# Optimization experiments

Measured on AMD Instinct MI355X. Metric: run time of the kernel, lower is better.

The kernel has to match this reference:

```python
import jax, jax.numpy as jnp
import numpy as np

# ---- config (matches init_kwargs) ----
B, N, D = 16, 300, 256
HEADS, HD = 8, D // 8
FF = 1024
HID = FF // 2                      # SwiGLU hidden
SPATIAL = [(80, 80), (40, 40), (20, 20), (10, 10)]
LVL = len(SPATIAL)
NP = 4                              # points per level
TP = LVL * NP                       # total sampling points = 16
L = sum(h * w for h, w in SPATIAL)  # 8400
EPS = 1e-6


def setup_inputs() -> dict:
    key = jax.random.key(0)
    ks = jax.random.split(key, 24)
    s = 0.02
    return {
        "target": jax.random.normal(ks[0], (B, N, D), jnp.float32),
        "reference_points": jax.random.uniform(ks[1], (B, N, 1, 4), jnp.float32, 0.05, 0.95),
        "memory": jax.random.normal(ks[2], (B, L, D), jnp.float32),
        # self-attention
        "qkv_w": jax.random.normal(ks[3], (3 * D, D), jnp.float32) * s,
        "qkv_b": jnp.zeros((3 * D,), jnp.float32),
        "out_w": jax.random.normal(ks[4], (D, D), jnp.float32) * s,
        "out_b": jnp.zeros((D,), jnp.float32),
        "norm1_w": jnp.ones((D,), jnp.float32),
        # deformable cross-attention
        "off_w": jax.random.normal(ks[5], (HEADS * TP * 2, D), jnp.float32) * s,
        "off_b": jax.random.normal(ks[6], (HEADS * TP * 2,), jnp.float32) * 0.1,
        "aw_w": jax.random.normal(ks[7], (HEADS * TP, D), jnp.float32) * s,
        "aw_b": jnp.zeros((HEADS * TP,), jnp.float32),
        "cout_w": jax.random.normal(ks[8], (D, D), jnp.float32) * s,
        "cout_b": jnp.zeros((D,), jnp.float32),
        "norm2_w": jnp.ones((D,), jnp.float32),
        # SwiGLU FFN
        "w13": jax.random.normal(ks[9], (2 * HID, D), jnp.float32) * s,
        "w13_b": jnp.zeros((2 * HID,), jnp.float32),
        "w2": jax.random.normal(ks[10], (D, HID), jnp.float32) * s,
        "w2_b": jnp.zeros((D,), jnp.float32),
        "norm3_w": jnp.ones((D,), jnp.float32),
    }


def rmsnorm(x, w):
    return x * jax.lax.rsqrt(jnp.mean(x * x, axis=-1, keepdims=True) + EPS) * w


def bilinear_sample(vflat, loc, H, W):
    """vflat: (BH, hd, H*W); loc: (BH, Q, 2) in [0,1]. grid_sample align_corners=False, zero pad."""
    x = loc[..., 0] * W - 0.5
    y = loc[..., 1] * H - 0.5
    x0 = jnp.floor(x); y0 = jnp.floor(y)
    dx = x - x0; dy = y - y0
    x0i = x0.astype(jnp.int32); y0i = y0.astype(jnp.int32)

    def gather(xi, yi, w):
        valid = (xi >= 0) & (xi < W) & (yi >= 0) & (yi < H)
        idx = jnp.clip(yi, 0, H - 1) * W + jnp.clip(xi, 0, W - 1)
        g = jnp.take_along_axis(vflat, idx[:, None, :], axis=2)  # (BH, hd, Q)
        return g * (w * valid)[:, None, :]

    return (gather(x0i, y0i, (1 - dx) * (1 - dy))
            + gather(x0i + 1, y0i, dx * (1 - dy))
            + gather(x0i, y0i + 1, (1 - dx) * dy)
            + gather(x0i + 1, y0i + 1, dx * dy))


def reference(target, reference_points, memory, qkv_w, qkv_b, out_w, out_b, norm1_w,
              off_w, off_b, aw_w, aw_b, cout_w, cout_b, norm2_w,
              w13, w13_b, w2, w2_b, norm3_w):
    # ---------- self-attention (query_pos_embed=None, attn_mask=None) ----------
    qkv = target @ qkv_w.T + qkv_b                    # (B,N,3D)
    qkv = qkv.reshape(B, N, 3, HEADS, HD).transpose(2, 0, 3, 1, 4)
    q, k, v = qkv[0], qkv[1], qkv[2]                  # (B,H,N,hd)
    attn = jax.nn.softmax(jnp.einsum("bhqd,bhkd->bhqk", q, k) / np.sqrt(HD), axis=-1)
    sa = jnp.einsum("bhqk,bhkd->bhqd", attn, v).transpose(0, 2, 1, 3).reshape(B, N, D)
    x = rmsnorm(target + (sa @ out_w.T + out_b), norm1_w)

    # ---------- deformable cross-attention ----------
    # value_op: memory -> per-head value (B,H,hd,L)
    val = memory.reshape(B, L, HEADS, HD).transpose(0, 2, 3, 1).reshape(B * HEADS, HD, L)

    offsets = (x @ off_w.T + off_b).reshape(B, N, HEADS, TP, 2)
    aw = jax.nn.softmax((x @ aw_w.T + aw_b).reshape(B, N, HEADS, TP), axis=-1)

    ref_xy = reference_points[:, :, :, None, :2]      # (B,N,1,1,2)
    ref_wh = reference_points[:, :, :, None, 2:]
    pts_scale = 1.0 / NP
    loc = ref_xy + offsets * pts_scale * ref_wh * 0.5  # (B,N,H,TP,2)
    loc = loc.transpose(0, 2, 1, 3, 4).reshape(B * HEADS, N, TP, 2)

    sampled = []
    start = 0
    for li, (H, W) in enumerate(SPATIAL):
        v_l = jax.lax.dynamic_slice_in_dim(val, start, H * W, axis=2)
        loc_l = loc[:, :, li * NP:(li + 1) * NP, :].reshape(B * HEADS, N * NP, 2)
        s = bilinear_sample(v_l, loc_l, H, W).reshape(B * HEADS, HD, N, NP)
        sampled.append(s)
        start += H * W
    sampled = jnp.concatenate(sampled, axis=-1)        # (BH, hd, N, TP)

    w = aw.transpose(0, 2, 1, 3).reshape(B * HEADS, 1, N, TP)
    ca = (sampled * w).sum(-1)                         # (BH, hd, N)
    ca = ca.reshape(B, HEADS, HD, N).transpose(0, 3, 1, 2).reshape(B, N, D)
    ca = ca @ cout_w.T + cout_b

    x = rmsnorm(x + ca, norm2_w)

    # ---------- SwiGLU FFN ----------
    h = x @ w13.T + w13_b
    h1, h2 = h[..., :HID], h[..., HID:]
    ffn = (jax.nn.silu(h1) * h2) @ w2.T + w2_b
    x = jnp.clip(x + ffn, -65504.0, 65504.0)
    return rmsnorm(x, norm3_w)
```

## Files before the change

kernel.cpp:

```cpp
#include <hip/hip_runtime.h>
#include <cstdint>
#include <cstddef>


typedef __attribute__((ext_vector_type(8))) short bf16x8;
typedef __attribute__((ext_vector_type(4))) float f32x4;

__device__ __forceinline__ unsigned short f2bf(float f) {
  unsigned int u = __float_as_uint(f);
  u = (u + 0x7fffu + ((u >> 16) & 1u)) >> 16;
  return (unsigned short)u;
}
__device__ __forceinline__ float bf2f(unsigned short b) {
  return __uint_as_float(((unsigned int)b) << 16);
}
__device__ __forceinline__ unsigned int pack2bf(float lo, float hi) {
  return ((unsigned int)f2bf(hi) << 16) | (unsigned int)f2bf(lo);
}

__device__ __forceinline__ void gemm_dev(
    const float* __restrict__ A, const float* __restrict__ W,
    const float* __restrict__ bias, float* __restrict__ C,
    int N, int K, int row0, int col0,
    unsigned short* As, unsigned short* Ws)
{
  const int t = threadIdx.x, wave = t >> 6, lane = t & 63;
  const int lr = lane & 15, g = lane >> 4;
  const int sr = t >> 4, sc = (t & 15) * 4;

  float4 ra[4], rw[8];
  const float* Ab = A + (size_t)(row0 + sr) * K + sc;
  const float* Wb = W + (size_t)(col0 + sr) * K + sc;

#pragma unroll
  for (int i = 0; i < 4; ++i) ra[i] = *(const float4*)(Ab + (size_t)16 * i * K);
#pragma unroll
  for (int j = 0; j < 8; ++j) rw[j] = *(const float4*)(Wb + (size_t)16 * j * K);

  f32x4 acc[4][2] = {};

  for (int k0 = 0; k0 < K; k0 += 64) {
    __syncthreads();
#pragma unroll
    for (int i = 0; i < 4; ++i) {
      uint2 p;
      p.x = pack2bf(ra[i].x, ra[i].y);
      p.y = pack2bf(ra[i].z, ra[i].w);
      *(uint2*)&As[(sr + 16 * i) * 72 + sc] = p;
    }
#pragma unroll
    for (int j = 0; j < 8; ++j) {
      uint2 p;
      p.x = pack2bf(rw[j].x, rw[j].y);
      p.y = pack2bf(rw[j].z, rw[j].w);
      *(uint2*)&Ws[(sr + 16 * j) * 72 + sc] = p;
    }
    __syncthreads();

    if (k0 + 64 < K) {
#pragma unroll
      for (int i = 0; i < 4; ++i)
        ra[i] = *(const float4*)(Ab + (size_t)16 * i * K + k0 + 64);
#pragma unroll
      for (int j = 0; j < 8; ++j)
        rw[j] = *(const float4*)(Wb + (size_t)16 * j * K + k0 + 64);
    }

#pragma unroll
    for (int ks = 0; ks < 2; ++ks) {
      bf16x8 aA[4], bB[2];
#pragma unroll
      for (int i = 0; i < 4; ++i)
        aA[i] = *(const bf16x8*)&As[(i * 16 + lr) * 72 + ks * 32 + g * 8];
#pragma unroll
      for (int j = 0; j < 2; ++j)
        bB[j] = *(const bf16x8*)&Ws[(wave * 32 + j * 16 + lr) * 72 + ks * 32 + g * 8];
#pragma unroll
      for (int i = 0; i < 4; ++i)
#pragma unroll
        for (int j = 0; j < 2; ++j)
          acc[i][j] = __builtin_amdgcn_mfma_f32_16x16x32_bf16(aA[i], bB[j], acc[i][j], 0, 0, 0);
    }
  }

  const float b0 = bias[col0 + wave * 32 + lr];
  const float b1 = bias[col0 + wave * 32 + 16 + lr];
#pragma unroll
  for (int i = 0; i < 4; ++i) {
#pragma unroll
    for (int r = 0; r < 4; ++r) {
      const int row = row0 + i * 16 + g * 4 + r;
      float* dst = &C[(size_t)row * N + col0 + wave * 32 + lr];
      dst[0]  = acc[i][0][r] + b0;
      dst[16] = acc[i][1][r] + b1;
    }
  }
}

__global__ __launch_bounds__(256) void gemm_mfma(
    const float* __restrict__ A, const float* __restrict__ W,
    const float* __restrict__ bias, float* __restrict__ C, int N, int K)
{
  __shared__ __align__(16) unsigned short As[64 * 72];
  __shared__ __align__(16) unsigned short Ws[128 * 72];
  gemm_dev(A, W, bias, C, N, K, blockIdx.y * 64, blockIdx.x * 128, As, Ws);
}

__global__ __launch_bounds__(256) void gemm_offaw(
    const float* __restrict__ X,
    const float* __restrict__ off_w, const float* __restrict__ off_b, float* __restrict__ OF,
    const float* __restrict__ aw_w, const float* __restrict__ aw_b, float* __restrict__ AW,
    int K)
{
  __shared__ __align__(16) unsigned short As[64 * 72];
  __shared__ __align__(16) unsigned short Ws[128 * 72];
  if (blockIdx.x < 2)
    gemm_dev(X, off_w, off_b, OF, 256, K, blockIdx.y * 64, blockIdx.x * 128, As, Ws);
  else
    gemm_dev(X, aw_w, aw_b, AW, 128, K, blockIdx.y * 64, 0, As, Ws);
}

__global__ __launch_bounds__(256) void repack_qkv(
    const float* __restrict__ qkv,
    unsigned short* __restrict__ Qb, unsigned short* __restrict__ Kb,
    unsigned short* __restrict__ VTb)
{
  const int bh = blockIdx.x, b = bh >> 3, h = bh & 7;
  const int half = blockIdx.y;
  const int t = threadIdx.x;
  const size_t base = (size_t)b * 300 * 768 + (size_t)h * 32;
  const float scale = 0.17677669529663687f;

  for (int i = t; i < 152 * 16; i += 256) {
    const int n = half * 152 + (i >> 4), cp = (i & 15) * 2;
    float2 q = make_float2(0.f, 0.f), k = make_float2(0.f, 0.f);
    if (n < 300) {
      q = *(const float2*)&qkv[base + (size_t)n * 768 + cp];
      k = *(const float2*)&qkv[base + (size_t)n * 768 + 256 + cp];
    }
    *(unsigned int*)&Qb[((size_t)bh * 304 + n) * 32 + cp] = pack2bf(q.x * scale, q.y * scale);
    *(unsigned int*)&Kb[((size_t)bh * 304 + n) * 32 + cp] = pack2bf(k.x, k.y);
  }
  for (int c = half * 16; c < half * 16 + 16; ++c) {
    for (int n = t; n < 320; n += 256) {
      float v = (n < 300) ? qkv[base + (size_t)n * 768 + 512 + c] : 0.f;
      VTb[((size_t)bh * 32 + c) * 320 + n] = f2bf(v);
    }
  }
}

__global__ __launch_bounds__(64) void attn_core(
    const unsigned short* __restrict__ Qb, const unsigned short* __restrict__ Kb,
    const unsigned short* __restrict__ VTb, float* __restrict__ sa)
{
  __shared__ __align__(16) unsigned short P[16 * 40];
  const int gt = blockIdx.x;
  const int bh = blockIdx.y, b = bh >> 3, h = bh & 7;
  const int lane = threadIdx.x, lr = lane & 15, g = lane >> 4;

  const unsigned short* Kbase = Kb + (size_t)bh * 304 * 32;
  const unsigned short* Vbase = VTb + (size_t)bh * 32 * 320;

  bf16x8 aQ = *(const bf16x8*)&Qb[((size_t)bh * 304 + gt * 16 + lr) * 32 + g * 8];

  f32x4 s[19];
  const f32x4 zero = {0.f, 0.f, 0.f, 0.f};
#pragma unroll
  for (int kt = 0; kt < 19; ++kt) {
    bf16x8 bK = *(const bf16x8*)&Kbase[(kt * 16 + lr) * 32 + g * 8];
    s[kt] = __builtin_amdgcn_mfma_f32_16x16x32_bf16(aQ, bK, zero, 0, 0, 0);
  }
  if (lr >= 12) {
    s[18][0] = -1e30f; s[18][1] = -1e30f; s[18][2] = -1e30f; s[18][3] = -1e30f;
  }

  float inv[4];
#pragma unroll
  for (int r = 0; r < 4; ++r) {
    float m = -1e30f;
#pragma unroll
    for (int kt = 0; kt < 19; ++kt) m = fmaxf(m, s[kt][r]);
#pragma unroll
    for (int o = 8; o >= 1; o >>= 1) m = fmaxf(m, __shfl_xor(m, o));
    float sum = 0.f;
#pragma unroll
    for (int kt = 0; kt < 19; ++kt) {
      float e = __expf(s[kt][r] - m);
      s[kt][r] = e;
      sum += e;
    }
#pragma unroll
    for (int o = 8; o >= 1; o >>= 1) sum += __shfl_xor(sum, o);
    inv[r] = 1.f / sum;
  }

  f32x4 o0 = {0.f, 0.f, 0.f, 0.f}, o1 = {0.f, 0.f, 0.f, 0.f};
#pragma unroll
  for (int ks = 0; ks < 10; ++ks) {
#pragma unroll
    for (int tp = 0; tp < 2; ++tp) {
      const int kt = ks * 2 + tp;
#pragma unroll
      for (int r = 0; r < 4; ++r) {
        unsigned short pv = (kt < 19) ? f2bf(s[kt][r]) : (unsigned short)0;
        P[(g * 4 + r) * 40 + tp * 16 + lr] = pv;
      }
    }
    asm volatile("s_waitcnt lgkmcnt(0)" ::: "memory");
    __builtin_amdgcn_sched_barrier(0);
    bf16x8 aP = *(const bf16x8*)&P[lr * 40 + g * 8];
    bf16x8 bV0 = *(const bf16x8*)&Vbase[(size_t)lr * 320 + ks * 32 + g * 8];
    bf16x8 bV1 = *(const bf16x8*)&Vbase[(size_t)(16 + lr) * 320 + ks * 32 + g * 8];
    o0 = __builtin_amdgcn_mfma_f32_16x16x32_bf16(aP, bV0, o0, 0, 0, 0);
    o1 = __builtin_amdgcn_mfma_f32_16x16x32_bf16(aP, bV1, o1, 0, 0, 0);
  }

#pragma unroll
  for (int r = 0; r < 4; ++r) {
    const int q = gt * 16 + g * 4 + r;
    if (q < 300) {
      const float iv = inv[r];
      float* dst = &sa[((size_t)b * 300 + q) * 256 + h * 32];
      dst[lr] = o0[r] * iv;
      dst[16 + lr] = o1[r] * iv;
    }
  }
}

__global__ __launch_bounds__(256) void add_rmsnorm(
    const float* __restrict__ a, const float* __restrict__ bsrc,
    const float* __restrict__ w, float* __restrict__ out, int clip)
{
  __shared__ float red[4];
  const int row = blockIdx.x, t = threadIdx.x;
  const size_t idx = (size_t)row * 256 + t;
  float v = a[idx] + bsrc[idx];
  if (clip) v = fminf(fmaxf(v, -65504.f), 65504.f);
  float s = v * v;
#pragma unroll
  for (int o = 32; o; o >>= 1) s += __shfl_xor(s, o);
  if ((t & 63) == 0) red[t >> 6] = s;
  __syncthreads();
  float tot = red[0] + red[1] + red[2] + red[3];
  out[idx] = v * rsqrtf(tot * (1.0f / 256.0f) + 1e-6f) * w[t];
}

__global__ __launch_bounds__(256) void swiglu_k(
    const float* __restrict__ h, float* __restrict__ hid)
{
  size_t i = (size_t)blockIdx.x * 256 + threadIdx.x;
  int row = (int)(i >> 9), c = (int)(i & 511);
  float a = h[(size_t)row * 1024 + c];
  float g = h[(size_t)row * 1024 + 512 + c];
  hid[i] = a / (1.f + __expf(-a)) * g;
}

__global__ __launch_bounds__(256) void deform_k(
    const float* __restrict__ memory, const float* __restrict__ refp,
    const float* __restrict__ OFF, const float* __restrict__ AW,
    float* __restrict__ ca)
{
  __shared__ float locx[8][16], locy[8][16], wgt[8][16];
  const int bn = blockIdx.x, b = bn / 300, t = threadIdx.x;

  if (t < 128) {
    int h = t >> 4, p = t & 15;
    float cx = refp[(size_t)bn * 4 + 0], cy = refp[(size_t)bn * 4 + 1];
    float rw = refp[(size_t)bn * 4 + 2], rh = refp[(size_t)bn * 4 + 3];
    float ox = OFF[(size_t)bn * 256 + h * 32 + p * 2 + 0];
    float oy = OFF[(size_t)bn * 256 + h * 32 + p * 2 + 1];
    locx[h][p] = cx + ox * 0.125f * rw;
    locy[h][p] = cy + oy * 0.125f * rh;
    float av = AW[(size_t)bn * 128 + t];
    float mx = av;
#pragma unroll
    for (int o = 8; o; o >>= 1) mx = fmaxf(mx, __shfl_xor(mx, o));
    float e = __expf(av - mx);
    float ssum = e;
#pragma unroll
    for (int o = 8; o; o >>= 1) ssum += __shfl_xor(ssum, o);
    wgt[h][p] = e / ssum;
  }
  __syncthreads();

  const int h = t >> 5, hd = t & 31;
  const float* mb = memory + (size_t)b * 8500 * 256 + h * 32 + hd;
  float acc = 0.f;
#pragma unroll
  for (int p = 0; p < 16; ++p) {
    const int HWs[4] = {80, 40, 20, 10};
    const int Sts[4] = {0, 6400, 8000, 8400};
    const int li = p >> 2;
    const int Hh = HWs[li], Ww = HWs[li], st = Sts[li];
    float x = locx[h][p] * (float)Ww - 0.5f;
    float y = locy[h][p] * (float)Hh - 0.5f;
    float x0f = floorf(x), y0f = floorf(y);
    float dx = x - x0f, dy = y - y0f;
    int x0 = (int)x0f, y0 = (int)y0f;
    float awp = wgt[h][p];
#pragma unroll
    for (int cc = 0; cc < 4; ++cc) {
      int xi = x0 + (cc & 1), yi = y0 + (cc >> 1);
      float wc = ((cc & 1) ? dx : 1.f - dx) * ((cc >> 1) ? dy : 1.f - dy);
      bool valid = (xi >= 0) && (xi < Ww) && (yi >= 0) && (yi < Hh);
      int xc = xi < 0 ? 0 : (xi >= Ww ? Ww - 1 : xi);
      int yc = yi < 0 ? 0 : (yi >= Hh ? Hh - 1 : yi);
      float gv = mb[(size_t)(st + yc * Ww + xc) * 256];
      acc += gv * (valid ? wc * awp : 0.f);
    }
  }
  ca[(size_t)bn * 256 + t] = acc;
}

extern "C" void kernel_launch(void* const* d_in, const int* in_sizes, int n_in,
                              void* d_out, int out_size, void* d_ws, size_t ws_size,
                              hipStream_t stream)
{
  (void)in_sizes; (void)n_in; (void)out_size; (void)ws_size;
  const float* target  = (const float*)d_in[0];
  const float* refp    = (const float*)d_in[1];
  const float* memory  = (const float*)d_in[2];
  const float* qkv_w   = (const float*)d_in[3];
  const float* qkv_b   = (const float*)d_in[4];
  const float* out_w   = (const float*)d_in[5];
  const float* out_b   = (const float*)d_in[6];
  const float* norm1_w = (const float*)d_in[7];
  const float* off_w   = (const float*)d_in[8];
  const float* off_b   = (const float*)d_in[9];
  const float* aw_w    = (const float*)d_in[10];
  const float* aw_b    = (const float*)d_in[11];
  const float* cout_w  = (const float*)d_in[12];
  const float* cout_b  = (const float*)d_in[13];
  const float* norm2_w = (const float*)d_in[14];
  const float* w13     = (const float*)d_in[15];
  const float* w13_b   = (const float*)d_in[16];
  const float* w2      = (const float*)d_in[17];
  const float* w2_b    = (const float*)d_in[18];
  const float* norm3_w = (const float*)d_in[19];
  float* out = (float*)d_out;

  float* ws  = (float*)d_ws;
  float* QKV = ws;
  float* SA  = QKV + 4800 * 768;
  float* T1  = SA  + 4800 * 256;
  float* X   = T1  + 4800 * 256;
  float* OF  = X   + 4800 * 256;
  float* AWb = OF  + 4800 * 256;
  float* CA  = AWb + 4800 * 128;
  float* X2  = CA  + 4800 * 256;
  float* Hb  = X2  + 4800 * 256;
  float* HID = Hb  + 4800 * 1024;

  unsigned short* Qb  = (unsigned short*)Hb;
  unsigned short* Kb  = Qb + 128 * 304 * 32;
  unsigned short* VTb = Kb + 128 * 304 * 32;

  dim3 blk(256);

  gemm_mfma<<<dim3(6, 75), blk, 0, stream>>>(target, qkv_w, qkv_b, QKV, 768, 256);
  repack_qkv<<<dim3(128, 2), blk, 0, stream>>>(QKV, Qb, Kb, VTb);
  attn_core<<<dim3(19, 128), dim3(64), 0, stream>>>(Qb, Kb, VTb, SA);
  gemm_mfma<<<dim3(2, 75), blk, 0, stream>>>(SA, out_w, out_b, T1, 256, 256);
  add_rmsnorm<<<4800, blk, 0, stream>>>(target, T1, norm1_w, X, 0);
  gemm_offaw<<<dim3(3, 75), blk, 0, stream>>>(X, off_w, off_b, OF, aw_w, aw_b, AWb, 256);
  deform_k<<<4800, blk, 0, stream>>>(memory, refp, OF, AWb, CA);
  gemm_mfma<<<dim3(2, 75), blk, 0, stream>>>(CA, cout_w, cout_b, T1, 256, 256);
  add_rmsnorm<<<4800, blk, 0, stream>>>(X, T1, norm2_w, X2, 0);
  gemm_mfma<<<dim3(8, 75), blk, 0, stream>>>(X2, w13, w13_b, Hb, 1024, 256);
  swiglu_k<<<9600, blk, 0, stream>>>(Hb, HID);
  gemm_mfma<<<dim3(2, 75), blk, 0, stream>>>(HID, w2, w2_b, T1, 256, 512);
  add_rmsnorm<<<4800, blk, 0, stream>>>(X2, T1, norm3_w, out, 1);
}
```

Before: 144.6 us.

## Fuse QKV repack into GEMM epilogue and SwiGLU into down-projection prologue

The QKV projection GEMM now writes bf16 Q (pre-scaled), K and transposed V directly in the per-head layout the attention kernel expects, with padding zeroed, so the fp32 QKV buffer and the separate repack kernel go away. The SwiGLU activation is computed while loading the A tile of the down-projection GEMM, which removes the standalone swiglu kernel and its HID intermediate. This cuts two launches and several full-size global round trips. In exchange, the Q/K epilogue does scattered 2-byte stores, and the fused GEMM reads twice as much A data per tile and recomputes the activation once per column block.

```diff
diff --git a/kernel.cpp b/kernel.cpp
--- a/kernel.cpp
+++ b/kernel.cpp
@@ -10,9 +10,6 @@
   unsigned int u = __float_as_uint(f);
   u = (u + 0x7fffu + ((u >> 16) & 1u)) >> 16;
   return (unsigned short)u;
-}
-__device__ __forceinline__ float bf2f(unsigned short b) {
-  return __uint_as_float(((unsigned int)b) << 16);
 }
 __device__ __forceinline__ unsigned int pack2bf(float lo, float hi) {
   return ((unsigned int)f2bf(hi) << 16) | (unsigned int)f2bf(lo);
@@ -120,31 +117,218 @@
     gemm_dev(X, aw_w, aw_b, AW, 128, K, blockIdx.y * 64, 0, As, Ws);
 }
 
-__global__ __launch_bounds__(256) void repack_qkv(
-    const float* __restrict__ qkv,
+__global__ __launch_bounds__(256) void gemm_qkv(
+    const float* __restrict__ A, const float* __restrict__ W,
+    const float* __restrict__ bias,
     unsigned short* __restrict__ Qb, unsigned short* __restrict__ Kb,
     unsigned short* __restrict__ VTb)
 {
-  const int bh = blockIdx.x, b = bh >> 3, h = bh & 7;
-  const int half = blockIdx.y;
-  const int t = threadIdx.x;
-  const size_t base = (size_t)b * 300 * 768 + (size_t)h * 32;
+  __shared__ __align__(16) unsigned short As[64 * 72];
+  __shared__ __align__(16) unsigned short Ws[128 * 72];
+  const int K = 256;
+  const int t = threadIdx.x, wave = t >> 6, lane = t & 63;
+  const int lr = lane & 15, g = lane >> 4;
+  const int row0 = blockIdx.y * 64, col0 = blockIdx.x * 128;
+  const int sr = t >> 4, sc = (t & 15) * 4;
+
+  float4 ra[4], rw[8];
+  const float* Ab = A + (size_t)(row0 + sr) * K + sc;
+  const float* Wb = W + (size_t)(col0 + sr) * K + sc;
+
+#pragma unroll
+  for (int i = 0; i < 4; ++i) ra[i] = *(const float4*)(Ab + (size_t)16 * i * K);
+#pragma unroll
+  for (int j = 0; j < 8; ++j) rw[j] = *(const float4*)(Wb + (size_t)16 * j * K);
+
+  f32x4 acc[4][2] = {};
+
+  for (int k0 = 0; k0 < K; k0 += 64) {
+    __syncthreads();
+#pragma unroll
+    for (int i = 0; i < 4; ++i) {
+      uint2 p;
+      p.x = pack2bf(ra[i].x, ra[i].y);
+      p.y = pack2bf(ra[i].z, ra[i].w);
+      *(uint2*)&As[(sr + 16 * i) * 72 + sc] = p;
+    }
+#pragma unroll
+    for (int j = 0; j < 8; ++j) {
+      uint2 p;
+      p.x = pack2bf(rw[j].x, rw[j].y);
+      p.y = pack2bf(rw[j].z, rw[j].w);
+      *(uint2*)&Ws[(sr + 16 * j) * 72 + sc] = p;
+    }
+    __syncthreads();
+
+    if (k0 + 64 < K) {
+#pragma unroll
+      for (int i = 0; i < 4; ++i)
+        ra[i] = *(const float4*)(Ab + (size_t)16 * i * K + k0 + 64);
+#pragma unroll
+      for (int j = 0; j < 8; ++j)
+        rw[j] = *(const float4*)(Wb + (size_t)16 * j * K + k0 + 64);
+    }
+
+#pragma unroll
+    for (int ks = 0; ks < 2; ++ks) {
+      bf16x8 aA[4], bB[2];
+#pragma unroll
+      for (int i = 0; i < 4; ++i)
+        aA[i] = *(const bf16x8*)&As[(i * 16 + lr) * 72 + ks * 32 + g * 8];
+#pragma unroll
+      for (int j = 0; j < 2; ++j)
+        bB[j] = *(const bf16x8*)&Ws[(wave * 32 + j * 16 + lr) * 72 + ks * 32 + g * 8];
+#pragma unroll
+      for (int i = 0; i < 4; ++i)
+#pragma unroll
+        for (int j = 0; j < 2; ++j)
+          acc[i][j] = __builtin_amdgcn_mfma_f32_16x16x32_bf16(aA[i], bB[j], acc[i][j], 0, 0, 0);
+    }
+  }
+
+  const int bx = blockIdx.x;
   const float scale = 0.17677669529663687f;
-
-  for (int i = t; i < 152 * 16; i += 256) {
-    const int n = half * 152 + (i >> 4), cp = (i & 15) * 2;
-    float2 q = make_float2(0.f, 0.f), k = make_float2(0.f, 0.f);
-    if (n < 300) {
-      q = *(const float2*)&qkv[base + (size_t)n * 768 + cp];
-      k = *(const float2*)&qkv[base + (size_t)n * 768 + 256 + cp];
-    }
-    *(unsigned int*)&Qb[((size_t)bh * 304 + n) * 32 + cp] = pack2bf(q.x * scale, q.y * scale);
-    *(unsigned int*)&Kb[((size_t)bh * 304 + n) * 32 + cp] = pack2bf(k.x, k.y);
-  }
-  for (int c = half * 16; c < half * 16 + 16; ++c) {
-    for (int n = t; n < 320; n += 256) {
-      float v = (n < 300) ? qkv[base + (size_t)n * 768 + 512 + c] : 0.f;
-      VTb[((size_t)bh * 32 + c) * 320 + n] = f2bf(v);
+  const float b0 = bias[col0 + wave * 32 + lr];
+  const float b1 = bias[col0 + wave * 32 + 16 + lr];
+
+  if (bx < 4) {
+    unsigned short* dstT = (bx < 2) ? Qb : Kb;
+    const float mul = (bx < 2) ? scale : 1.0f;
+#pragma unroll
+    for (int i = 0; i < 4; ++i) {
+#pragma unroll
+      for (int r = 0; r < 4; ++r) {
+        const int row = row0 + i * 16 + g * 4 + r;
+        const int b = row / 300, n = row - b * 300;
+#pragma unroll
+        for (int j = 0; j < 2; ++j) {
+          const int c768 = col0 + wave * 32 + j * 16 + lr;
+          const int h = (c768 >> 5) & 7, c = c768 & 31;
+          const float v = (acc[i][j][r] + (j ? b1 : b0)) * mul;
+          dstT[((size_t)(b * 8 + h) * 304 + n) * 32 + c] = f2bf(v);
+        }
+      }
+    }
+  } else {
+    __syncthreads();
+#pragma unroll
+    for (int i = 0; i < 4; ++i)
+#pragma unroll
+      for (int r = 0; r < 4; ++r)
+#pragma unroll
+        for (int j = 0; j < 2; ++j) {
+          const int c_local = wave * 32 + j * 16 + lr;
+          const int n_local = i * 16 + g * 4 + r;
+          Ws[c_local * 72 + n_local] = f2bf(acc[i][j][r] + (j ? b1 : b0));
+        }
+    __syncthreads();
+    for (int idx = t; idx < 128 * 64; idx += 256) {
+      const int c_local = idx >> 6, n_local = idx & 63;
+      const int row = row0 + n_local;
+      const int b = row / 300, n = row - b * 300;
+      const int c768 = col0 + c_local;
+      const int h = (c768 >> 5) & 7, c = c768 & 31;
+      VTb[((size_t)(b * 8 + h) * 32 + c) * 320 + n] = Ws[c_local * 72 + n_local];
+    }
+    if (blockIdx.y == 74) {
+      for (int idx = t; idx < 64 * 32 * 20; idx += 256) {
+        const int n = 300 + idx % 20;
+        const int rem = idx / 20;
+        const int c = rem & 31, bh4 = rem >> 5;
+        const int b = bh4 >> 2, h = (bx - 4) * 4 + (bh4 & 3);
+        VTb[((size_t)(b * 8 + h) * 32 + c) * 320 + n] = 0;
+      }
+    }
+  }
+}
+
+__global__ __launch_bounds__(256) void gemm_swiglu(
+    const float* __restrict__ Hb, const float* __restrict__ W,
+    const float* __restrict__ bias, float* __restrict__ C)
+{
+  __shared__ __align__(16) unsigned short As[64 * 72];
+  __shared__ __align__(16) unsigned short Ws[128 * 72];
+  const int K = 512, N = 256;
+  const int t = threadIdx.x, wave = t >> 6, lane = t & 63;
+  const int lr = lane & 15, g = lane >> 4;
+  const int row0 = blockIdx.y * 64, col0 = blockIdx.x * 128;
+  const int sr = t >> 4, sc = (t & 15) * 4;
+
+  float4 ra1[4], ra2[4], rw[8];
+  const float* Ab = Hb + (size_t)(row0 + sr) * 1024 + sc;
+  const float* Wb = W + (size_t)(col0 + sr) * K + sc;
+
+#pragma unroll
+  for (int i = 0; i < 4; ++i) {
+    ra1[i] = *(const float4*)(Ab + (size_t)16 * i * 1024);
+    ra2[i] = *(const float4*)(Ab + (size_t)16 * i * 1024 + 512);
+  }
+#pragma unroll
+  for (int j = 0; j < 8; ++j) rw[j] = *(const float4*)(Wb + (size_t)16 * j * K);
+
+  f32x4 acc[4][2] = {};
+
+  for (int k0 = 0; k0 < K; k0 += 64) {
+    __syncthreads();
+#pragma unroll
+    for (int i = 0; i < 4; ++i) {
+      float4 v;
+      v.x = ra1[i].x / (1.f + __expf(-ra1[i].x)) * ra2[i].x;
+      v.y = ra1[i].y / (1.f + __expf(-ra1[i].y)) * ra2[i].y;
+      v.z = ra1[i].z / (1.f + __expf(-ra1[i].z)) * ra2[i].z;
+      v.w = ra1[i].w / (1.f + __expf(-ra1[i].w)) * ra2[i].w;
+      uint2 p;
+      p.x = pack2bf(v.x, v.y);
+      p.y = pack2bf(v.z, v.w);
+      *(uint2*)&As[(sr + 16 * i) * 72 + sc] = p;
+    }
+#pragma unroll
+    for (int j = 0; j < 8; ++j) {
+      uint2 p;
+      p.x = pack2bf(rw[j].x, rw[j].y);
+      p.y = pack2bf(rw[j].z, rw[j].w);
+      *(uint2*)&Ws[(sr + 16 * j) * 72 + sc] = p;
+    }
+    __syncthreads();
+
+    if (k0 + 64 < K) {
+#pragma unroll
+      for (int i = 0; i < 4; ++i) {
+        ra1[i] = *(const float4*)(Ab + (size_t)16 * i * 1024 + k0 + 64);
+        ra2[i] = *(const float4*)(Ab + (size_t)16 * i * 1024 + 512 + k0 + 64);
+      }
+#pragma unroll
+      for (int j = 0; j < 8; ++j)
+        rw[j] = *(const float4*)(Wb + (size_t)16 * j * K + k0 + 64);
+    }
+
+#pragma unroll
+    for (int ks = 0; ks < 2; ++ks) {
+      bf16x8 aA[4], bB[2];
+#pragma unroll
+      for (int i = 0; i < 4; ++i)
+        aA[i] = *(const bf16x8*)&As[(i * 16 + lr) * 72 + ks * 32 + g * 8];
+#pragma unroll
+      for (int j = 0; j < 2; ++j)
+        bB[j] = *(const bf16x8*)&Ws[(wave * 32 + j * 16 + lr) * 72 + ks * 32 + g * 8];
+#pragma unroll
+      for (int i = 0; i < 4; ++i)
+#pragma unroll
+        for (int j = 0; j < 2; ++j)
+          acc[i][j] = __builtin_amdgcn_mfma_f32_16x16x32_bf16(aA[i], bB[j], acc[i][j], 0, 0, 0);
+    }
+  }
+
+  const float b0 = bias[col0 + wave * 32 + lr];
+  const float b1 = bias[col0 + wave * 32 + 16 + lr];
+#pragma unroll
+  for (int i = 0; i < 4; ++i) {
+#pragma unroll
+    for (int r = 0; r < 4; ++r) {
+      const int row = row0 + i * 16 + g * 4 + r;
+      float* dst = &C[(size_t)row * N + col0 + wave * 32 + lr];
+      dst[0]  = acc[i][0][r] + b0;
+      dst[16] = acc[i][1][r] + b1;
     }
   }
 }
@@ -243,16 +427,6 @@
   __syncthreads();
   float tot = red[0] + red[1] + red[2] + red[3];
   out[idx] = v * rsqrtf(tot * (1.0f / 256.0f) + 1e-6f) * w[t];
-}
-
-__global__ __launch_bounds__(256) void swiglu_k(
-    const float* __restrict__ h, float* __restrict__ hid)
-{
-  size_t i = (size_t)blockIdx.x * 256 + threadIdx.x;
-  int row = (int)(i >> 9), c = (int)(i & 511);
-  float a = h[(size_t)row * 1024 + c];
-  float g = h[(size_t)row * 1024 + 512 + c];
-  hid[i] = a / (1.f + __expf(-a)) * g;
 }
 
 __global__ __launch_bounds__(256) void deform_k(
@@ -340,8 +514,7 @@
   float* out = (float*)d_out;
 
   float* ws  = (float*)d_ws;
-  float* QKV = ws;
-  float* SA  = QKV + 4800 * 768;
+  float* SA  = ws;
   float* T1  = SA  + 4800 * 256;
   float* X   = T1  + 4800 * 256;
   float* OF  = X   + 4800 * 256;
@@ -349,16 +522,13 @@
   float* CA  = AWb + 4800 * 128;
   float* X2  = CA  + 4800 * 256;
   float* Hb  = X2  + 4800 * 256;
-  float* HID = Hb  + 4800 * 1024;
-
-  unsigned short* Qb  = (unsigned short*)Hb;
+  unsigned short* Qb  = (unsigned short*)(Hb + 4800 * 1024);
   unsigned short* Kb  = Qb + 128 * 304 * 32;
   unsigned short* VTb = Kb + 128 * 304 * 32;
 
   dim3 blk(256);
 
-  gemm_mfma<<<dim3(6, 75), blk, 0, stream>>>(target, qkv_w, qkv_b, QKV, 768, 256);
-  repack_qkv<<<dim3(128, 2), blk, 0, stream>>>(QKV, Qb, Kb, VTb);
+  gemm_qkv<<<dim3(6, 75), blk, 0, stream>>>(target, qkv_w, qkv_b, Qb, Kb, VTb);
   attn_core<<<dim3(19, 128), dim3(64), 0, stream>>>(Qb, Kb, VTb, SA);
   gemm_mfma<<<dim3(2, 75), blk, 0, stream>>>(SA, out_w, out_b, T1, 256, 256);
   add_rmsnorm<<<4800, blk, 0, stream>>>(target, T1, norm1_w, X, 0);
@@ -367,7 +537,6 @@
   gemm_mfma<<<dim3(2, 75), blk, 0, stream>>>(CA, cout_w, cout_b, T1, 256, 256);
   add_rmsnorm<<<4800, blk, 0, stream>>>(X, T1, norm2_w, X2, 0);
   gemm_mfma<<<dim3(8, 75), blk, 0, stream>>>(X2, w13, w13_b, Hb, 1024, 256);
-  swiglu_k<<<9600, blk, 0, stream>>>(Hb, HID);
-  gemm_mfma<<<dim3(2, 75), blk, 0, stream>>>(HID, w2, w2_b, T1, 256, 512);
+  gemm_swiglu<<<dim3(2, 75), blk, 0, stream>>>(Hb, w2, w2_b, T1);
   add_rmsnorm<<<4800, blk, 0, stream>>>(X2, T1, norm3_w, out, 1);
 }
```

Measured after the change: 136.3 us. -5.7%, faster.
